# Kernel optimization log

Hardware: AMD Instinct MI355X
Metric: run time of the kernel (lower is better)

The kernel has to match this reference:

```python
import jax, jax.numpy as jnp
import numpy as np

B, T, D = 65536, 100, 16   # batch, num_blocks (seq len), input_dim
HID = 64                    # MLP hidden dim
OUT = 2                     # output classes


def setup_inputs() -> dict:
    key = jax.random.key(0)
    ks = jax.random.split(key, 12)
    s_ih = 1.0  # pytorch LSTM init: U(-1/sqrt(hidden), 1/sqrt(hidden)), hidden=1
    inp = {
        "X":    jax.random.normal(ks[0], (B, T, D), dtype=jnp.float32),
        # LSTM (hidden_size=1), gate order i, f, g, o
        "W_ih": jax.random.uniform(ks[1], (4, D), jnp.float32, -s_ih, s_ih),
        "W_hh": jax.random.uniform(ks[2], (4, 1), jnp.float32, -s_ih, s_ih),
        "b_ih": jax.random.uniform(ks[3], (4,), jnp.float32, -s_ih, s_ih),
        "b_hh": jax.random.uniform(ks[4], (4,), jnp.float32, -s_ih, s_ih),
        # MLP head
        "W1": jax.random.uniform(ks[5], (HID, T), jnp.float32, -1/np.sqrt(T), 1/np.sqrt(T)),
        "b1": jax.random.uniform(ks[6], (HID,), jnp.float32, -1/np.sqrt(T), 1/np.sqrt(T)),
        "W2": jax.random.uniform(ks[7], (HID, HID), jnp.float32, -1/np.sqrt(HID), 1/np.sqrt(HID)),
        "b2": jax.random.uniform(ks[8], (HID,), jnp.float32, -1/np.sqrt(HID), 1/np.sqrt(HID)),
        "W3": jax.random.uniform(ks[9], (OUT, HID), jnp.float32, -1/np.sqrt(HID), 1/np.sqrt(HID)),
        "b3": jax.random.uniform(ks[10], (OUT,), jnp.float32, -1/np.sqrt(HID), 1/np.sqrt(HID)),
    }
    return inp


def _lstm_h1(X, W_ih, W_hh, b_ih, b_hh):
    # hidden_size = 1 LSTM, batch_first. Returns h sequence [B, T].
    b = b_ih + b_hh                                   # [4]
    x_proj = jnp.einsum('btd,gd->btg', X, W_ih) + b   # [B, T, 4] precomputed input projections
    x_proj = jnp.swapaxes(x_proj, 0, 1)               # [T, B, 4]
    w_hh = W_hh[:, 0]                                 # [4]

    def step(carry, xg):
        h, c = carry                                  # [B], [B]
        gates = xg + h[:, None] * w_hh                # [B, 4]
        i = jax.nn.sigmoid(gates[:, 0])
        f = jax.nn.sigmoid(gates[:, 1])
        g = jnp.tanh(gates[:, 2])
        o = jax.nn.sigmoid(gates[:, 3])
        c = f * c + i * g
        h = o * jnp.tanh(c)
        return (h, c), h

    init = (jnp.zeros((X.shape[0],), X.dtype), jnp.zeros((X.shape[0],), X.dtype))
    _, hs = jax.lax.scan(step, init, x_proj)          # hs: [T, B]
    return jnp.swapaxes(hs, 0, 1)                     # [B, T]


def reference(X, W_ih, W_hh, b_ih, b_hh, W1, b1, W2, b2, W3, b3):
    h = _lstm_h1(X, W_ih, W_hh, b_ih, b_hh)           # [B, T]
    y = jax.nn.relu(h) @ W1.T + b1                    # [B, HID]
    y = jax.nn.relu(y) @ W2.T + b2                    # [B, HID]
    y = jax.nn.relu(y) @ W3.T + b3                    # [B, OUT]
    return jax.nn.log_softmax(y, axis=1)
```

## Files before the change

kernel.cpp:

```cpp
#include <hip/hip_runtime.h>
#include <math.h>

#define NB     65536
#define TSTEPS 100
#define DDIM   16
#define HID    64

__device__ __forceinline__ float fsigmoid(float x) {
    return 1.0f / (1.0f + __expf(-x));
}
__device__ __forceinline__ float ftanh(float x) {
    float a = fabsf(x);
    float t = __expf(-2.0f * a);
    float r = (1.0f - t) / (1.0f + t);
    return copysignf(r, x);
}

#define LOADPAIR(BUF, P) do {                                              \
    _Pragma("unroll")                                                      \
    for (int q = 0; q < 8; ++q) {                                          \
        float4 v = xp[(P) * 8 + q];                                        \
        BUF[4*q+0] = v.x; BUF[4*q+1] = v.y;                                \
        BUF[4*q+2] = v.z; BUF[4*q+3] = v.w;                                \
    } } while (0)

#define PROCPAIR(BUF, T0) do {                                             \
    _Pragma("unroll")                                                      \
    for (int s = 0; s < 2; ++s) {                                          \
        float g0 = fmaf(h, wh0, gb0);                                      \
        float g1 = fmaf(h, wh1, gb1);                                      \
        float g2 = fmaf(h, wh2, gb2);                                      \
        float g3 = fmaf(h, wh3, gb3);                                      \
        _Pragma("unroll")                                                  \
        for (int d = 0; d < 16; ++d) {                                     \
            float xv = BUF[s * 16 + d];                                    \
            g0 = fmaf(xv, wih[d],      g0);                                \
            g1 = fmaf(xv, wih[16 + d], g1);                                \
            g2 = fmaf(xv, wih[32 + d], g2);                                \
            g3 = fmaf(xv, wih[48 + d], g3);                                \
        }                                                                  \
        float ig = fsigmoid(g0);                                           \
        float fg = fsigmoid(g1);                                           \
        float gg = ftanh(g2);                                              \
        float og = fsigmoid(g3);                                           \
        c = fmaf(fg, c, ig * gg);                                          \
        h = og * ftanh(c);                                                 \
        float rh = fmaxf(h, 0.0f);                                         \
        const int tcur = (T0) + s;                                         \
        _Pragma("unroll")                                                  \
        for (int q = 0; q < 16; ++q) {                                     \
            float4 w = *reinterpret_cast<const float4*>(                   \
                           &sW1T[tcur * HID + 4 * q]);                     \
            y1[4*q+0] = fmaf(rh, w.x, y1[4*q+0]);                          \
            y1[4*q+1] = fmaf(rh, w.y, y1[4*q+1]);                          \
            y1[4*q+2] = fmaf(rh, w.z, y1[4*q+2]);                          \
            y1[4*q+3] = fmaf(rh, w.w, y1[4*q+3]);                          \
        }                                                                  \
    } } while (0)

__global__ void __launch_bounds__(256, 1)
lstm_mlp_fused(const float* __restrict__ X,
               const float* __restrict__ W_ih,
               const float* __restrict__ W_hh,
               const float* __restrict__ b_ih,
               const float* __restrict__ b_hh,
               const float* __restrict__ W1,
               const float* __restrict__ b1,
               const float* __restrict__ W2,
               const float* __restrict__ b2,
               const float* __restrict__ W3,
               const float* __restrict__ b3,
               float* __restrict__ out)
{
    __shared__ __align__(16) float sW1T[TSTEPS * HID];
    __shared__ __align__(16) float sW2[HID * HID];
    __shared__ __align__(16) float sW3[2 * HID];
    __shared__ __align__(16) float sB1[HID];
    __shared__ __align__(16) float sB2[HID];
    __shared__ __align__(16) float sWih[4 * DDIM];
    __shared__ float sMisc[12];

    const int tid = threadIdx.x;
    for (int i = tid; i < TSTEPS * HID; i += 256) {
        int j = i / TSTEPS;
        int t = i - j * TSTEPS;
        sW1T[t * HID + j] = W1[i];
    }
    for (int i = tid; i < HID * HID; i += 256) sW2[i] = W2[i];
    if (tid < 2 * HID) sW3[tid] = W3[tid];
    if (tid < HID) { sB1[tid] = b1[tid]; sB2[tid] = b2[tid]; }
    if (tid < 4 * DDIM) sWih[tid] = W_ih[tid];
    if (tid < 4) { sMisc[tid] = b_ih[tid] + b_hh[tid]; sMisc[4 + tid] = W_hh[tid]; }
    if (tid < 2) sMisc[8 + tid] = b3[tid];
    __syncthreads();

    float wih[64];
    #pragma unroll
    for (int q = 0; q < 16; ++q) {
        float4 v = *reinterpret_cast<const float4*>(&sWih[4 * q]);
        wih[4*q+0] = v.x; wih[4*q+1] = v.y; wih[4*q+2] = v.z; wih[4*q+3] = v.w;
    }
    const float gb0 = sMisc[0], gb1 = sMisc[1], gb2 = sMisc[2], gb3 = sMisc[3];
    const float wh0 = sMisc[4], wh1 = sMisc[5], wh2 = sMisc[6], wh3 = sMisc[7];
    const float bo0 = sMisc[8], bo1 = sMisc[9];

    const int b = blockIdx.x * 256 + tid;
    const float4* __restrict__ xp =
        reinterpret_cast<const float4*>(X + (size_t)b * (TSTEPS * DDIM));

    float y1[HID];
    #pragma unroll
    for (int q = 0; q < 16; ++q) {
        float4 v = *reinterpret_cast<const float4*>(&sB1[4 * q]);
        y1[4*q+0] = v.x; y1[4*q+1] = v.y; y1[4*q+2] = v.z; y1[4*q+3] = v.w;
    }

    float h = 0.0f, c = 0.0f;
    float bufA[32], bufB[32];

    LOADPAIR(bufA, 0);
    for (int it = 0; it < 25; ++it) {
        LOADPAIR(bufB, 2 * it + 1);
        PROCPAIR(bufA, 4 * it);
        if (it < 24) LOADPAIR(bufA, 2 * it + 2);
        PROCPAIR(bufB, 4 * it + 2);
    }

    #pragma unroll
    for (int j = 0; j < HID; ++j) y1[j] = fmaxf(y1[j], 0.0f);

    float o0 = bo0, o1 = bo1;
    for (int k = 0; k < HID; ++k) {
        float acc = sB2[k];
        #pragma unroll
        for (int q = 0; q < 16; ++q) {
            float4 w = *reinterpret_cast<const float4*>(&sW2[k * HID + 4 * q]);
            acc = fmaf(y1[4*q+0], w.x, acc);
            acc = fmaf(y1[4*q+1], w.y, acc);
            acc = fmaf(y1[4*q+2], w.z, acc);
            acc = fmaf(y1[4*q+3], w.w, acc);
        }
        acc = fmaxf(acc, 0.0f);
        o0 = fmaf(acc, sW3[k], o0);
        o1 = fmaf(acc, sW3[HID + k], o1);
    }

    float m = fmaxf(o0, o1);
    float lse = m + __logf(__expf(o0 - m) + __expf(o1 - m));
    float2 res = make_float2(o0 - lse, o1 - lse);
    reinterpret_cast<float2*>(out)[b] = res;
}

extern "C" void kernel_launch(void* const* d_in, const int* in_sizes, int n_in,
                              void* d_out, int out_size, void* d_ws, size_t ws_size,
                              hipStream_t stream) {
    const float* X    = (const float*)d_in[0];
    const float* W_ih = (const float*)d_in[1];
    const float* W_hh = (const float*)d_in[2];
    const float* b_ih = (const float*)d_in[3];
    const float* b_hh = (const float*)d_in[4];
    const float* W1   = (const float*)d_in[5];
    const float* b1   = (const float*)d_in[6];
    const float* W2   = (const float*)d_in[7];
    const float* b2   = (const float*)d_in[8];
    const float* W3   = (const float*)d_in[9];
    const float* b3   = (const float*)d_in[10];
    float* out = (float*)d_out;

    lstm_mlp_fused<<<NB / 256, 256, 0, stream>>>(
        X, W_ih, W_hh, b_ih, b_hh, W1, b1, W2, b2, W3, b3, out);
}
```

Before: 582.5 us.

## Stage X through double-buffered LDS with coalesced loads, 128-thread blocks

Replaces per-thread strided float4 loads of each row's sequence with a cooperative load where 8 adjacent threads fetch one row's two-timestep chunk. The data is staged into a padded, double-buffered shared-memory tile and each thread then reads its own row from LDS. Block size drops from 256 to 128 to give 512 blocks, and W2, W3 and the biases are now read from global memory (cached) instead of shared memory. The aim is better global-memory coalescing and more blocks across the CUs. The cost is a __syncthreads on every one of the 50 chunks and uniform global loads in the MLP tail.

```diff
diff --git a/kernel.cpp b/kernel.cpp
--- a/kernel.cpp
+++ b/kernel.cpp
@@ -1,10 +1,12 @@
 #include <hip/hip_runtime.h>
 #include <math.h>
 
-#define NB     65536
-#define TSTEPS 100
-#define DDIM   16
-#define HID    64
+#define NB      65536
+#define TSTEPS  100
+#define DDIM    16
+#define HID     64
+#define ROWS    128
+#define LDSROW  36
 
 __device__ __forceinline__ float fsigmoid(float x) {
     return 1.0f / (1.0f + __expf(-x));
@@ -12,53 +14,10 @@
 __device__ __forceinline__ float ftanh(float x) {
     float a = fabsf(x);
     float t = __expf(-2.0f * a);
-    float r = (1.0f - t) / (1.0f + t);
-    return copysignf(r, x);
+    return copysignf((1.0f - t) / (1.0f + t), x);
 }
 
-#define LOADPAIR(BUF, P) do {                                              \
-    _Pragma("unroll")                                                      \
-    for (int q = 0; q < 8; ++q) {                                          \
-        float4 v = xp[(P) * 8 + q];                                        \
-        BUF[4*q+0] = v.x; BUF[4*q+1] = v.y;                                \
-        BUF[4*q+2] = v.z; BUF[4*q+3] = v.w;                                \
-    } } while (0)
-
-#define PROCPAIR(BUF, T0) do {                                             \
-    _Pragma("unroll")                                                      \
-    for (int s = 0; s < 2; ++s) {                                          \
-        float g0 = fmaf(h, wh0, gb0);                                      \
-        float g1 = fmaf(h, wh1, gb1);                                      \
-        float g2 = fmaf(h, wh2, gb2);                                      \
-        float g3 = fmaf(h, wh3, gb3);                                      \
-        _Pragma("unroll")                                                  \
-        for (int d = 0; d < 16; ++d) {                                     \
-            float xv = BUF[s * 16 + d];                                    \
-            g0 = fmaf(xv, wih[d],      g0);                                \
-            g1 = fmaf(xv, wih[16 + d], g1);                                \
-            g2 = fmaf(xv, wih[32 + d], g2);                                \
-            g3 = fmaf(xv, wih[48 + d], g3);                                \
-        }                                                                  \
-        float ig = fsigmoid(g0);                                           \
-        float fg = fsigmoid(g1);                                           \
-        float gg = ftanh(g2);                                              \
-        float og = fsigmoid(g3);                                           \
-        c = fmaf(fg, c, ig * gg);                                          \
-        h = og * ftanh(c);                                                 \
-        float rh = fmaxf(h, 0.0f);                                         \
-        const int tcur = (T0) + s;                                         \
-        _Pragma("unroll")                                                  \
-        for (int q = 0; q < 16; ++q) {                                     \
-            float4 w = *reinterpret_cast<const float4*>(                   \
-                           &sW1T[tcur * HID + 4 * q]);                     \
-            y1[4*q+0] = fmaf(rh, w.x, y1[4*q+0]);                          \
-            y1[4*q+1] = fmaf(rh, w.y, y1[4*q+1]);                          \
-            y1[4*q+2] = fmaf(rh, w.z, y1[4*q+2]);                          \
-            y1[4*q+3] = fmaf(rh, w.w, y1[4*q+3]);                          \
-        }                                                                  \
-    } } while (0)
-
-__global__ void __launch_bounds__(256, 1)
+__global__ void __launch_bounds__(128, 1)
 lstm_mlp_fused(const float* __restrict__ X,
                const float* __restrict__ W_ih,
                const float* __restrict__ W_hh,
@@ -73,82 +32,133 @@
                float* __restrict__ out)
 {
     __shared__ __align__(16) float sW1T[TSTEPS * HID];
-    __shared__ __align__(16) float sW2[HID * HID];
-    __shared__ __align__(16) float sW3[2 * HID];
+    __shared__ __align__(16) float sX[2][ROWS * LDSROW];
+    __shared__ __align__(16) float sWih[4 * DDIM];
     __shared__ __align__(16) float sB1[HID];
-    __shared__ __align__(16) float sB2[HID];
-    __shared__ __align__(16) float sWih[4 * DDIM];
-    __shared__ float sMisc[12];
+    __shared__ float sMisc[8];
 
     const int tid = threadIdx.x;
-    for (int i = tid; i < TSTEPS * HID; i += 256) {
+
+    for (int i = tid; i < TSTEPS * HID; i += 128) {
         int j = i / TSTEPS;
         int t = i - j * TSTEPS;
         sW1T[t * HID + j] = W1[i];
     }
-    for (int i = tid; i < HID * HID; i += 256) sW2[i] = W2[i];
-    if (tid < 2 * HID) sW3[tid] = W3[tid];
-    if (tid < HID) { sB1[tid] = b1[tid]; sB2[tid] = b2[tid]; }
     if (tid < 4 * DDIM) sWih[tid] = W_ih[tid];
+    if (tid < HID)      sB1[tid]  = b1[tid];
     if (tid < 4) { sMisc[tid] = b_ih[tid] + b_hh[tid]; sMisc[4 + tid] = W_hh[tid]; }
-    if (tid < 2) sMisc[8 + tid] = b3[tid];
+
+    const int row0 = blockIdx.x * ROWS;
+    const float4* __restrict__ xg = reinterpret_cast<const float4*>(X) + (size_t)row0 * 400;
+    const int srow = tid >> 3;
+    const int scol = tid & 7;
+
+    float4 st[8];
+    #pragma unroll
+    for (int it = 0; it < 8; ++it)
+        st[it] = xg[(size_t)(it * 16 + srow) * 400 + scol];
+    #pragma unroll
+    for (int it = 0; it < 8; ++it)
+        *reinterpret_cast<float4*>(&sX[0][(it * 16 + srow) * LDSROW + scol * 4]) = st[it];
     __syncthreads();
 
     float wih[64];
     #pragma unroll
     for (int q = 0; q < 16; ++q) {
         float4 v = *reinterpret_cast<const float4*>(&sWih[4 * q]);
-        wih[4*q+0] = v.x; wih[4*q+1] = v.y; wih[4*q+2] = v.z; wih[4*q+3] = v.w;
+        wih[4*q] = v.x; wih[4*q+1] = v.y; wih[4*q+2] = v.z; wih[4*q+3] = v.w;
     }
     const float gb0 = sMisc[0], gb1 = sMisc[1], gb2 = sMisc[2], gb3 = sMisc[3];
     const float wh0 = sMisc[4], wh1 = sMisc[5], wh2 = sMisc[6], wh3 = sMisc[7];
-    const float bo0 = sMisc[8], bo1 = sMisc[9];
-
-    const int b = blockIdx.x * 256 + tid;
-    const float4* __restrict__ xp =
-        reinterpret_cast<const float4*>(X + (size_t)b * (TSTEPS * DDIM));
 
     float y1[HID];
     #pragma unroll
     for (int q = 0; q < 16; ++q) {
         float4 v = *reinterpret_cast<const float4*>(&sB1[4 * q]);
-        y1[4*q+0] = v.x; y1[4*q+1] = v.y; y1[4*q+2] = v.z; y1[4*q+3] = v.w;
+        y1[4*q] = v.x; y1[4*q+1] = v.y; y1[4*q+2] = v.z; y1[4*q+3] = v.w;
     }
 
     float h = 0.0f, c = 0.0f;
-    float bufA[32], bufB[32];
 
-    LOADPAIR(bufA, 0);
-    for (int it = 0; it < 25; ++it) {
-        LOADPAIR(bufB, 2 * it + 1);
-        PROCPAIR(bufA, 4 * it);
-        if (it < 24) LOADPAIR(bufA, 2 * it + 2);
-        PROCPAIR(bufB, 4 * it + 2);
+    for (int ch = 0; ch < 50; ++ch) {
+        if (ch < 49) {
+            #pragma unroll
+            for (int it = 0; it < 8; ++it)
+                st[it] = xg[(size_t)(it * 16 + srow) * 400 + (ch + 1) * 8 + scol];
+        }
+
+        float xr[32];
+        const float* mysX = &sX[ch & 1][tid * LDSROW];
+        #pragma unroll
+        for (int q = 0; q < 8; ++q) {
+            float4 v = *reinterpret_cast<const float4*>(&mysX[4 * q]);
+            xr[4*q] = v.x; xr[4*q+1] = v.y; xr[4*q+2] = v.z; xr[4*q+3] = v.w;
+        }
+
+        #pragma unroll
+        for (int s = 0; s < 2; ++s) {
+            float g0 = fmaf(h, wh0, gb0);
+            float g1 = fmaf(h, wh1, gb1);
+            float g2 = fmaf(h, wh2, gb2);
+            float g3 = fmaf(h, wh3, gb3);
+            #pragma unroll
+            for (int d = 0; d < 16; ++d) {
+                float xv = xr[s * 16 + d];
+                g0 = fmaf(xv, wih[d],      g0);
+                g1 = fmaf(xv, wih[16 + d], g1);
+                g2 = fmaf(xv, wih[32 + d], g2);
+                g3 = fmaf(xv, wih[48 + d], g3);
+            }
+            float ig = fsigmoid(g0);
+            float fg = fsigmoid(g1);
+            float gg = ftanh(g2);
+            float og = fsigmoid(g3);
+            c = fmaf(fg, c, ig * gg);
+            h = og * ftanh(c);
+            float rh = fmaxf(h, 0.0f);
+            const float* w1row = &sW1T[(2 * ch + s) * HID];
+            #pragma unroll
+            for (int q = 0; q < 16; ++q) {
+                float4 w = *reinterpret_cast<const float4*>(&w1row[4 * q]);
+                y1[4*q]   = fmaf(rh, w.x, y1[4*q]);
+                y1[4*q+1] = fmaf(rh, w.y, y1[4*q+1]);
+                y1[4*q+2] = fmaf(rh, w.z, y1[4*q+2]);
+                y1[4*q+3] = fmaf(rh, w.w, y1[4*q+3]);
+            }
+        }
+
+        if (ch < 49) {
+            float* dst = &sX[(ch + 1) & 1][0];
+            #pragma unroll
+            for (int it = 0; it < 8; ++it)
+                *reinterpret_cast<float4*>(&dst[(it * 16 + srow) * LDSROW + scol * 4]) = st[it];
+        }
+        __syncthreads();
     }
 
     #pragma unroll
     for (int j = 0; j < HID; ++j) y1[j] = fmaxf(y1[j], 0.0f);
 
-    float o0 = bo0, o1 = bo1;
+    float o0 = b3[0], o1 = b3[1];
     for (int k = 0; k < HID; ++k) {
-        float acc = sB2[k];
+        float acc = b2[k];
+        const float4* w2row = reinterpret_cast<const float4*>(W2 + k * HID);
         #pragma unroll
         for (int q = 0; q < 16; ++q) {
-            float4 w = *reinterpret_cast<const float4*>(&sW2[k * HID + 4 * q]);
-            acc = fmaf(y1[4*q+0], w.x, acc);
+            float4 w = w2row[q];
+            acc = fmaf(y1[4*q],   w.x, acc);
             acc = fmaf(y1[4*q+1], w.y, acc);
             acc = fmaf(y1[4*q+2], w.z, acc);
             acc = fmaf(y1[4*q+3], w.w, acc);
         }
         acc = fmaxf(acc, 0.0f);
-        o0 = fmaf(acc, sW3[k], o0);
-        o1 = fmaf(acc, sW3[HID + k], o1);
+        o0 = fmaf(acc, W3[k], o0);
+        o1 = fmaf(acc, W3[HID + k], o1);
     }
 
     float m = fmaxf(o0, o1);
     float lse = m + __logf(__expf(o0 - m) + __expf(o1 - m));
-    float2 res = make_float2(o0 - lse, o1 - lse);
-    reinterpret_cast<float2*>(out)[b] = res;
+    reinterpret_cast<float2*>(out)[row0 + tid] = make_float2(o0 - lse, o1 - lse);
 }
 
 extern "C" void kernel_launch(void* const* d_in, const int* in_sizes, int n_in,
@@ -167,6 +177,6 @@
     const float* b3   = (const float*)d_in[10];
     float* out = (float*)d_out;
 
-    lstm_mlp_fused<<<NB / 256, 256, 0, stream>>>(
+    lstm_mlp_fused<<<NB / ROWS, ROWS, 0, stream>>>(
         X, W_ih, W_hh, b_ih, b_hh, W1, b1, W2, b2, W3, b3, out);
 }
```

After: 599.5 us. 2.9% more time.

## Deepen X prefetch to four buffers and read W2/W3 from global memory

Applied to the files above, without the earlier changes.

Replaces the two-buffer X prefetch with four register buffers so that two pairs of timesteps are in flight while computing, and marks the main loop unroll 1. It also drops the shared-memory copies of W2, W3, b2 and b3, reading them directly from global memory with uniform addresses that can become scalar loads. This is meant to hide more global-load latency in the memory-bound recurrence and cut LDS use and setup. The cost is higher register pressure from the 128 buffered floats, which may cause spills.

```diff
diff --git a/kernel.cpp b/kernel.cpp
--- a/kernel.cpp
+++ b/kernel.cpp
@@ -1,10 +1,10 @@
 #include <hip/hip_runtime.h>
 #include <math.h>
 
-#define NB     65536
-#define TSTEPS 100
-#define DDIM   16
-#define HID    64
+#define NB      65536
+#define TSTEPS  100
+#define DDIM    16
+#define HID     64
 
 __device__ __forceinline__ float fsigmoid(float x) {
     return 1.0f / (1.0f + __expf(-x));
@@ -12,8 +12,7 @@
 __device__ __forceinline__ float ftanh(float x) {
     float a = fabsf(x);
     float t = __expf(-2.0f * a);
-    float r = (1.0f - t) / (1.0f + t);
-    return copysignf(r, x);
+    return copysignf((1.0f - t) / (1.0f + t), x);
 }
 
 #define LOADPAIR(BUF, P) do {                                              \
@@ -46,11 +45,10 @@
         c = fmaf(fg, c, ig * gg);                                          \
         h = og * ftanh(c);                                                 \
         float rh = fmaxf(h, 0.0f);                                         \
-        const int tcur = (T0) + s;                                         \
+        const float* w1row = &sW1T[((T0) + s) * HID];   \
         _Pragma("unroll")                                                  \
         for (int q = 0; q < 16; ++q) {                                     \
-            float4 w = *reinterpret_cast<const float4*>(                   \
-                           &sW1T[tcur * HID + 4 * q]);                     \
+            float4 w = *reinterpret_cast<const float4*>(&w1row[4 * q]);    \
             y1[4*q+0] = fmaf(rh, w.x, y1[4*q+0]);                          \
             y1[4*q+1] = fmaf(rh, w.y, y1[4*q+1]);                          \
             y1[4*q+2] = fmaf(rh, w.z, y1[4*q+2]);                          \
@@ -73,12 +71,9 @@
                float* __restrict__ out)
 {
     __shared__ __align__(16) float sW1T[TSTEPS * HID];
-    __shared__ __align__(16) float sW2[HID * HID];
-    __shared__ __align__(16) float sW3[2 * HID];
+    __shared__ __align__(16) float sWih[4 * DDIM];
     __shared__ __align__(16) float sB1[HID];
-    __shared__ __align__(16) float sB2[HID];
-    __shared__ __align__(16) float sWih[4 * DDIM];
-    __shared__ float sMisc[12];
+    __shared__ float sMisc[8];
 
     const int tid = threadIdx.x;
     for (int i = tid; i < TSTEPS * HID; i += 256) {
@@ -86,23 +81,19 @@
         int t = i - j * TSTEPS;
         sW1T[t * HID + j] = W1[i];
     }
-    for (int i = tid; i < HID * HID; i += 256) sW2[i] = W2[i];
-    if (tid < 2 * HID) sW3[tid] = W3[tid];
-    if (tid < HID) { sB1[tid] = b1[tid]; sB2[tid] = b2[tid]; }
     if (tid < 4 * DDIM) sWih[tid] = W_ih[tid];
+    if (tid < HID)      sB1[tid]  = b1[tid];
     if (tid < 4) { sMisc[tid] = b_ih[tid] + b_hh[tid]; sMisc[4 + tid] = W_hh[tid]; }
-    if (tid < 2) sMisc[8 + tid] = b3[tid];
     __syncthreads();
 
     float wih[64];
     #pragma unroll
     for (int q = 0; q < 16; ++q) {
         float4 v = *reinterpret_cast<const float4*>(&sWih[4 * q]);
-        wih[4*q+0] = v.x; wih[4*q+1] = v.y; wih[4*q+2] = v.z; wih[4*q+3] = v.w;
+        wih[4*q] = v.x; wih[4*q+1] = v.y; wih[4*q+2] = v.z; wih[4*q+3] = v.w;
     }
     const float gb0 = sMisc[0], gb1 = sMisc[1], gb2 = sMisc[2], gb3 = sMisc[3];
     const float wh0 = sMisc[4], wh1 = sMisc[5], wh2 = sMisc[6], wh3 = sMisc[7];
-    const float bo0 = sMisc[8], bo1 = sMisc[9];
 
     const int b = blockIdx.x * 256 + tid;
     const float4* __restrict__ xp =
@@ -112,43 +103,52 @@
     #pragma unroll
     for (int q = 0; q < 16; ++q) {
         float4 v = *reinterpret_cast<const float4*>(&sB1[4 * q]);
-        y1[4*q+0] = v.x; y1[4*q+1] = v.y; y1[4*q+2] = v.z; y1[4*q+3] = v.w;
+        y1[4*q] = v.x; y1[4*q+1] = v.y; y1[4*q+2] = v.z; y1[4*q+3] = v.w;
     }
 
     float h = 0.0f, c = 0.0f;
-    float bufA[32], bufB[32];
 
-    LOADPAIR(bufA, 0);
+    float A0[32], A1[32], B0[32], B1[32];
+    LOADPAIR(A0, 0); LOADPAIR(A1, 1); LOADPAIR(B0, 2); LOADPAIR(B1, 3);
+
+    #pragma unroll 1
     for (int it = 0; it < 25; ++it) {
-        LOADPAIR(bufB, 2 * it + 1);
-        PROCPAIR(bufA, 4 * it);
-        if (it < 24) LOADPAIR(bufA, 2 * it + 2);
-        PROCPAIR(bufB, 4 * it + 2);
+        if (it & 1) {
+            PROCPAIR(B0, 4 * it);
+            if (it < 23) LOADPAIR(B0, 2 * it + 4);
+            PROCPAIR(B1, 4 * it + 2);
+            if (it < 23) LOADPAIR(B1, 2 * it + 5);
+        } else {
+            PROCPAIR(A0, 4 * it);
+            if (it < 23) LOADPAIR(A0, 2 * it + 4);
+            PROCPAIR(A1, 4 * it + 2);
+            if (it < 23) LOADPAIR(A1, 2 * it + 5);
+        }
     }
 
     #pragma unroll
     for (int j = 0; j < HID; ++j) y1[j] = fmaxf(y1[j], 0.0f);
 
-    float o0 = bo0, o1 = bo1;
+    float o0 = b3[0], o1 = b3[1];
     for (int k = 0; k < HID; ++k) {
-        float acc = sB2[k];
+        float acc = b2[k];
+        const float4* w2row = reinterpret_cast<const float4*>(W2 + k * HID);
         #pragma unroll
         for (int q = 0; q < 16; ++q) {
-            float4 w = *reinterpret_cast<const float4*>(&sW2[k * HID + 4 * q]);
-            acc = fmaf(y1[4*q+0], w.x, acc);
+            float4 w = w2row[q];
+            acc = fmaf(y1[4*q],   w.x, acc);
             acc = fmaf(y1[4*q+1], w.y, acc);
             acc = fmaf(y1[4*q+2], w.z, acc);
             acc = fmaf(y1[4*q+3], w.w, acc);
         }
         acc = fmaxf(acc, 0.0f);
-        o0 = fmaf(acc, sW3[k], o0);
-        o1 = fmaf(acc, sW3[HID + k], o1);
+        o0 = fmaf(acc, W3[k], o0);
+        o1 = fmaf(acc, W3[HID + k], o1);
     }
 
     float m = fmaxf(o0, o1);
     float lse = m + __logf(__expf(o0 - m) + __expf(o1 - m));
-    float2 res = make_float2(o0 - lse, o1 - lse);
-    reinterpret_cast<float2*>(out)[b] = res;
+    reinterpret_cast<float2*>(out)[b] = make_float2(o0 - lse, o1 - lse);
 }
 
 extern "C" void kernel_launch(void* const* d_in, const int* in_sizes, int n_in,
```

New measurement: 794.5 us. +36.4%, slower.
